# Kernel optimization log

Hardware: AMD Instinct MI355X
Metric: run time of the kernel (lower is better)

## Reference

```python
import jax, jax.numpy as jnp
import numpy as np

B, F = 512, 512
NUM_KERNEL, DIM_KERNEL = 50, 16


def setup_inputs() -> dict:
    key = jax.random.key(0)
    k1, k2 = jax.random.split(key)
    x = jax.random.normal(k1, (B, F), dtype=jnp.float32)
    # glorot-uniform-like scale for the learned kernel
    limit = (6.0 / (F + NUM_KERNEL * DIM_KERNEL)) ** 0.5
    W = jax.random.uniform(k2, (F, NUM_KERNEL * DIM_KERNEL), dtype=jnp.float32,
                           minval=-limit, maxval=limit)
    return {"x": x, "W": W}


def reference(x, W):
    # activation: (B, K, D)
    act = (x @ W).reshape(-1, NUM_KERNEL, DIM_KERNEL)
    # pairwise L1 over the kernel dim D: l1[b, b2, k] = sum_d |act[b,k,d] - act[b2,k,d]|
    diff = act[:, None, :, :] - act[None, :, :, :]      # (B, B, K, D)
    l1 = jnp.sum(jnp.abs(diff), axis=-1)                # (B, B, K)
    features = jnp.sum(jnp.exp(-l1), axis=1)            # (B, K), includes self-term (=1)
    return jnp.concatenate([x, features], axis=1)       # (B, F + K)
```

## Files before the change

kernel.cpp:

```cpp
#include <hip/hip_runtime.h>
#include <hip/hip_bf16.h>
#include <hip/hip_fp16.h>


#define B_ROWS 512
#define F_IN   512
#define NK     50
#define DK     16
#define N_COLS (NK * DK)
#define OUT_COLS (F_IN + NK)

#if __has_builtin(__builtin_amdgcn_exp2f)
#define EXP2F __builtin_amdgcn_exp2f
#else
#define EXP2F exp2f
#endif

typedef __attribute__((ext_vector_type(8))) short bf16x8;
typedef __attribute__((ext_vector_type(4))) float f32x4;

__device__ __forceinline__ short bfs(float f) {
    __hip_bfloat16 h = __float2bfloat16(f);
    return *reinterpret_cast<short*>(&h);
}

__global__ __launch_bounds__(256) void gemm_ksplit_kernel(const float* __restrict__ x,
                                                          const float* __restrict__ W,
                                                          float* __restrict__ act,
                                                          float* __restrict__ out) {
    __shared__ float red[4 * 64 * 8];

    const int tid = threadIdx.x;
    const int wave = tid >> 6, l = tid & 63;
    const int bid = blockIdx.y * 32 + blockIdx.x;

    if (bid < 128) {
        #pragma unroll
        for (int i = 0; i < 2; ++i) {
            int gid = bid * 512 + i * 256 + tid;
            int row = gid >> 7, c4 = gid & 127;
            float4 v = ((const float4*)x)[gid];
            float* o = out + row * OUT_COLS + c4 * 4;
            *(float2*)o = make_float2(v.x, v.y);
            *(float2*)(o + 2) = make_float2(v.z, v.w);
        }
    }

    const int mBase = blockIdx.x * 16;
    const int nBase = blockIdx.y * 32;
    const int rc = l & 15, kg = l >> 4;

    const float* pa = x + (mBase + rc) * F_IN + wave * 128 + kg * 8;
    const float* pb = W + (wave * 128 + kg * 8) * N_COLS + nBase + rc;

    f32x4 acc0 = {0.f, 0.f, 0.f, 0.f};
    f32x4 acc1 = {0.f, 0.f, 0.f, 0.f};

    #pragma unroll
    for (int ks = 0; ks < 4; ++ks) {
        float4 a0 = *(const float4*)(pa + ks * 32);
        float4 a1 = *(const float4*)(pa + ks * 32 + 4);
        bf16x8 a;
        a[0] = bfs(a0.x); a[1] = bfs(a0.y); a[2] = bfs(a0.z); a[3] = bfs(a0.w);
        a[4] = bfs(a1.x); a[5] = bfs(a1.y); a[6] = bfs(a1.z); a[7] = bfs(a1.w);

        const float* pk = pb + (ks * 32) * N_COLS;
        bf16x8 b0, b1;
        #pragma unroll
        for (int j = 0; j < 8; ++j) {
            b0[j] = bfs(pk[j * N_COLS]);
            b1[j] = bfs(pk[j * N_COLS + 16]);
        }
        acc0 = __builtin_amdgcn_mfma_f32_16x16x32_bf16(a, b0, acc0, 0, 0, 0);
        acc1 = __builtin_amdgcn_mfma_f32_16x16x32_bf16(a, b1, acc1, 0, 0, 0);
    }

    const int ro = (wave * 64 + l) * 8;
    *(f32x4*)(red + ro)     = acc0;
    *(f32x4*)(red + ro + 4) = acc1;
    __syncthreads();

    {
        const int e = tid * 2;
        const int le = e >> 3, j0 = e & 7;
        float2 s = make_float2(0.f, 0.f);
        #pragma unroll
        for (int w = 0; w < 4; ++w) {
            float2 v = *(const float2*)(red + w * 512 + e);
            s.x += v.x; s.y += v.y;
        }
        const int row = mBase + (le >> 4) * 4 + (j0 & 3);
        const int col = nBase + (le & 15) + (j0 >> 2) * 16;
        act[row * N_COLS + col]       = s.x;
        act[(row + 1) * N_COLS + col] = s.y;
    }
}

__global__ __launch_bounds__(256) void pairwise_h2_kernel(const float* __restrict__ act,
                                                          float* __restrict__ out) {
    const int k = blockIdx.x;
    const int chunk = blockIdx.y;
    __shared__ uint2 Ah4[B_ROWS * 4];

    const int tid = threadIdx.x;
    const float* base = act + k * DK;
    #pragma unroll
    for (int i = 0; i < 8; ++i) {
        int idx = tid + i * 256;
        int b = idx >> 2, d4 = idx & 3;
        float4 v = *(const float4*)(base + b * N_COLS + d4 * 4);
        __half2 h0 = __float22half2_rn(make_float2(v.x, v.y));
        __half2 h1 = __float22half2_rn(make_float2(v.z, v.w));
        uint2 u;
        u.x = __builtin_bit_cast(unsigned, h0);
        u.y = __builtin_bit_cast(unsigned, h1);
        Ah4[idx ^ ((idx >> 6) & 15)] = u;
    }
    __syncthreads();

    const int rt = tid >> 5;
    const int q = tid & 31;
    const int row0 = chunk * 32 + rt * 4;

    __half2 m[4][8];
    #pragma unroll
    for (int r = 0; r < 4; ++r) {
        int gr = row0 + r;
        int xr = (gr >> 4) & 15;
        #pragma unroll
        for (int j = 0; j < 4; ++j) {
            uint2 u = Ah4[(gr * 4 + j) ^ xr];
            m[r][2 * j]     = __builtin_bit_cast(__half2, u.x);
            m[r][2 * j + 1] = __builtin_bit_cast(__half2, u.y);
        }
    }

    const uint2* bq = Ah4 + q * 64;
    const int xm = q & 15;

    float acc[4] = {0.f, 0.f, 0.f, 0.f};
    #pragma unroll 4
    for (int i = 0; i < 16; ++i) {
        __half2 v[8];
        #pragma unroll
        for (int j = 0; j < 4; ++j) {
            uint2 u = bq[(i * 4 + j) ^ xm];
            v[2 * j]     = __builtin_bit_cast(__half2, u.x);
            v[2 * j + 1] = __builtin_bit_cast(__half2, u.y);
        }
        #pragma unroll
        for (int r = 0; r < 4; ++r) {
            __half2 s = __habs2(__hsub2(m[r][0], v[0]));
            #pragma unroll
            for (int jj = 1; jj < 8; ++jj)
                s = __hadd2(s, __habs2(__hsub2(m[r][jj], v[jj])));
            float2 f = __half22float2(s);
            acc[r] += EXP2F((f.x + f.y) * -1.4426950408889634f);
        }
    }

    #pragma unroll
    for (int r = 0; r < 4; ++r) {
        acc[r] += __shfl_xor(acc[r], 1);
        acc[r] += __shfl_xor(acc[r], 2);
        acc[r] += __shfl_xor(acc[r], 4);
        acc[r] += __shfl_xor(acc[r], 8);
        acc[r] += __shfl_xor(acc[r], 16);
    }
    if (q == 0) {
        #pragma unroll
        for (int r = 0; r < 4; ++r)
            out[(row0 + r) * OUT_COLS + F_IN + k] = acc[r];
    }
}

extern "C" void kernel_launch(void* const* d_in, const int* in_sizes, int n_in,
                              void* d_out, int out_size, void* d_ws, size_t ws_size,
                              hipStream_t stream) {
    const float* x = (const float*)d_in[0];
    const float* W = (const float*)d_in[1];
    float* out = (float*)d_out;
    float* act = (float*)d_ws;

    gemm_ksplit_kernel<<<dim3(32, 25), dim3(256), 0, stream>>>(x, W, act, out);
    pairwise_h2_kernel<<<dim3(50, 16), dim3(256), 0, stream>>>(act, out);
}
```

Baseline: 32.05 us.

## Fuse GEMM and pairwise kernels with ticket-based producer/consumer scheduling

Merges the two launches into a single persistent-style kernel. Blocks take tickets from a global atomic counter: the first 40 tickets compute larger 64x160 GEMM tiles over the full K (no k-split reduction) and write fp16 activations. Later tickets run the pairwise L1/exp work after spinning on per-column-group done counters. This removes one launch boundary, halves activation traffic by storing fp16, and lets the pairwise phase overlap with GEMM tail work. The cost is global atomics, spin-wait latency, bounded-spin correctness risk and much less GEMM parallelism (40 blocks).

```diff
diff --git a/kernel.cpp b/kernel.cpp
--- a/kernel.cpp
+++ b/kernel.cpp
@@ -9,6 +9,9 @@
 #define DK     16
 #define N_COLS (NK * DK)
 #define OUT_COLS (F_IN + NK)
+#define NBLOCKS 800
+#define NPROD   40
+#define POOL    (NPROD + NBLOCKS)
 
 #if __has_builtin(__builtin_amdgcn_exp2f)
 #define EXP2F __builtin_amdgcn_exp2f
@@ -19,102 +22,121 @@
 typedef __attribute__((ext_vector_type(8))) short bf16x8;
 typedef __attribute__((ext_vector_type(4))) float f32x4;
 
+__device__ unsigned long long g_ticket = 0;
+__device__ unsigned long long g_done[5] = {0, 0, 0, 0, 0};
+
 __device__ __forceinline__ short bfs(float f) {
     __hip_bfloat16 h = __float2bfloat16(f);
     return *reinterpret_cast<short*>(&h);
 }
 
-__global__ __launch_bounds__(256) void gemm_ksplit_kernel(const float* __restrict__ x,
-                                                          const float* __restrict__ W,
-                                                          float* __restrict__ act,
-                                                          float* __restrict__ out) {
-    __shared__ float red[4 * 64 * 8];
-
+__global__ __launch_bounds__(256) void fused_kernel(const float* __restrict__ x,
+                                                    const float* __restrict__ W,
+                                                    __half* __restrict__ act_h,
+                                                    float* __restrict__ out) {
+    __shared__ uint2 Ah4[2048];
+    __shared__ unsigned long long sTk;
+
+    const int bid = blockIdx.x;
     const int tid = threadIdx.x;
     const int wave = tid >> 6, l = tid & 63;
-    const int bid = blockIdx.y * 32 + blockIdx.x;
-
-    if (bid < 128) {
-        #pragma unroll
-        for (int i = 0; i < 2; ++i) {
-            int gid = bid * 512 + i * 256 + tid;
-            int row = gid >> 7, c4 = gid & 127;
-            float4 v = ((const float4*)x)[gid];
-            float* o = out + row * OUT_COLS + c4 * 4;
-            *(float2*)o = make_float2(v.x, v.y);
-            *(float2*)(o + 2) = make_float2(v.z, v.w);
-        }
-    }
-
-    const int mBase = blockIdx.x * 16;
-    const int nBase = blockIdx.y * 32;
     const int rc = l & 15, kg = l >> 4;
 
-    const float* pa = x + (mBase + rc) * F_IN + wave * 128 + kg * 8;
-    const float* pb = W + (wave * 128 + kg * 8) * N_COLS + nBase + rc;
-
-    f32x4 acc0 = {0.f, 0.f, 0.f, 0.f};
-    f32x4 acc1 = {0.f, 0.f, 0.f, 0.f};
-
-    #pragma unroll
-    for (int ks = 0; ks < 4; ++ks) {
-        float4 a0 = *(const float4*)(pa + ks * 32);
-        float4 a1 = *(const float4*)(pa + ks * 32 + 4);
-        bf16x8 a;
-        a[0] = bfs(a0.x); a[1] = bfs(a0.y); a[2] = bfs(a0.z); a[3] = bfs(a0.w);
-        a[4] = bfs(a1.x); a[5] = bfs(a1.y); a[6] = bfs(a1.z); a[7] = bfs(a1.w);
-
-        const float* pk = pb + (ks * 32) * N_COLS;
-        bf16x8 b0, b1;
-        #pragma unroll
-        for (int j = 0; j < 8; ++j) {
-            b0[j] = bfs(pk[j * N_COLS]);
-            b1[j] = bfs(pk[j * N_COLS + 16]);
-        }
-        acc0 = __builtin_amdgcn_mfma_f32_16x16x32_bf16(a, b0, acc0, 0, 0, 0);
-        acc1 = __builtin_amdgcn_mfma_f32_16x16x32_bf16(a, b1, acc1, 0, 0, 0);
-    }
-
-    const int ro = (wave * 64 + l) * 8;
-    *(f32x4*)(red + ro)     = acc0;
-    *(f32x4*)(red + ro + 4) = acc1;
+    unsigned long long epoch;
+    for (;;) {
+        __syncthreads();
+        if (tid == 0) sTk = atomicAdd(&g_ticket, 1ULL);
+        __syncthreads();
+        const unsigned long long t = sTk;
+        const unsigned r = (unsigned)(t % POOL);
+        if (r >= NPROD) { epoch = t / POOL; break; }
+
+        const int mc = r / 5, ncp = r % 5;
+        const int wm = (wave >> 1) & 1, wn = wave & 1;
+        const int rowb = mc * 64 + wm * 32;
+        const int colb = ncp * 160 + wn * 80;
+
+        const float* paw = x + (rowb + rc) * F_IN + kg * 8;
+        const float* pbw = W + (kg * 8) * N_COLS + colb + rc;
+
+        f32x4 acc[2][5] = {};
+        #pragma unroll 2
+        for (int ks = 0; ks < 16; ++ks) {
+            bf16x8 a[2];
+            #pragma unroll
+            for (int mf = 0; mf < 2; ++mf) {
+                float4 a0 = *(const float4*)(paw + mf * 16 * F_IN + ks * 32);
+                float4 a1 = *(const float4*)(paw + mf * 16 * F_IN + ks * 32 + 4);
+                a[mf][0] = bfs(a0.x); a[mf][1] = bfs(a0.y);
+                a[mf][2] = bfs(a0.z); a[mf][3] = bfs(a0.w);
+                a[mf][4] = bfs(a1.x); a[mf][5] = bfs(a1.y);
+                a[mf][6] = bfs(a1.z); a[mf][7] = bfs(a1.w);
+            }
+            const float* pk = pbw + ks * 32 * N_COLS;
+            #pragma unroll
+            for (int nf = 0; nf < 5; ++nf) {
+                bf16x8 b;
+                #pragma unroll
+                for (int j = 0; j < 8; ++j)
+                    b[j] = bfs(pk[j * N_COLS + nf * 16]);
+                acc[0][nf] = __builtin_amdgcn_mfma_f32_16x16x32_bf16(a[0], b, acc[0][nf], 0, 0, 0);
+                acc[1][nf] = __builtin_amdgcn_mfma_f32_16x16x32_bf16(a[1], b, acc[1][nf], 0, 0, 0);
+            }
+        }
+        #pragma unroll
+        for (int mf = 0; mf < 2; ++mf)
+            #pragma unroll
+            for (int nf = 0; nf < 5; ++nf)
+                #pragma unroll
+                for (int r4 = 0; r4 < 4; ++r4) {
+                    int row = rowb + mf * 16 + kg * 4 + r4;
+                    int col = colb + nf * 16 + rc;
+                    act_h[row * N_COLS + col] = __float2half(acc[mf][nf][r4]);
+                }
+
+        if (ncp == 0) {
+            #pragma unroll
+            for (int i = 0; i < 32; ++i) {
+                int idx = tid + i * 256;
+                int rr = idx >> 7, c4 = idx & 127;
+                float4 v = *(const float4*)(x + (mc * 64 + rr) * F_IN + c4 * 4);
+                float* o = out + (mc * 64 + rr) * OUT_COLS + c4 * 4;
+                *(float2*)o = make_float2(v.x, v.y);
+                *(float2*)(o + 2) = make_float2(v.z, v.w);
+            }
+        }
+
+        __syncthreads();
+        if (tid == 0) {
+            __builtin_amdgcn_fence(__ATOMIC_RELEASE, "");
+            __hip_atomic_fetch_add(&g_done[ncp], 1ULL,
+                                   __ATOMIC_RELAXED, __HIP_MEMORY_SCOPE_SYSTEM);
+        }
+    }
+
+    const int k = bid >> 4;
+    const int chunk = bid & 15;
+    const int nc = k / 10;
+    const unsigned long long target = 8ULL * (epoch + 1);
+
+    if (tid == 0) {
+        for (int it = 0; it < 3000000; ++it) {
+            if (__hip_atomic_load(&g_done[nc], __ATOMIC_RELAXED,
+                                  __HIP_MEMORY_SCOPE_SYSTEM) >= target) break;
+        }
+    }
     __syncthreads();
+    __builtin_amdgcn_fence(__ATOMIC_ACQUIRE, "");
 
     {
-        const int e = tid * 2;
-        const int le = e >> 3, j0 = e & 7;
-        float2 s = make_float2(0.f, 0.f);
-        #pragma unroll
-        for (int w = 0; w < 4; ++w) {
-            float2 v = *(const float2*)(red + w * 512 + e);
-            s.x += v.x; s.y += v.y;
-        }
-        const int row = mBase + (le >> 4) * 4 + (j0 & 3);
-        const int col = nBase + (le & 15) + (j0 >> 2) * 16;
-        act[row * N_COLS + col]       = s.x;
-        act[(row + 1) * N_COLS + col] = s.y;
-    }
-}
-
-__global__ __launch_bounds__(256) void pairwise_h2_kernel(const float* __restrict__ act,
-                                                          float* __restrict__ out) {
-    const int k = blockIdx.x;
-    const int chunk = blockIdx.y;
-    __shared__ uint2 Ah4[B_ROWS * 4];
-
-    const int tid = threadIdx.x;
-    const float* base = act + k * DK;
-    #pragma unroll
-    for (int i = 0; i < 8; ++i) {
-        int idx = tid + i * 256;
-        int b = idx >> 2, d4 = idx & 3;
-        float4 v = *(const float4*)(base + b * N_COLS + d4 * 4);
-        __half2 h0 = __float22half2_rn(make_float2(v.x, v.y));
-        __half2 h1 = __float22half2_rn(make_float2(v.z, v.w));
-        uint2 u;
-        u.x = __builtin_bit_cast(unsigned, h0);
-        u.y = __builtin_bit_cast(unsigned, h1);
-        Ah4[idx ^ ((idx >> 6) & 15)] = u;
+        const __half* base = act_h + k * DK;
+        #pragma unroll
+        for (int i = 0; i < 8; ++i) {
+            int idx = tid + i * 256;
+            int b = idx >> 2, d4 = idx & 3;
+            uint2 u = *(const uint2*)(base + b * N_COLS + d4 * 4);
+            Ah4[idx ^ ((idx >> 6) & 15)] = u;
+        }
     }
     __syncthreads();
 
@@ -180,8 +202,7 @@
     const float* x = (const float*)d_in[0];
     const float* W = (const float*)d_in[1];
     float* out = (float*)d_out;
-    float* act = (float*)d_ws;
-
-    gemm_ksplit_kernel<<<dim3(32, 25), dim3(256), 0, stream>>>(x, W, act, out);
-    pairwise_h2_kernel<<<dim3(50, 16), dim3(256), 0, stream>>>(act, out);
+    __half* act_h = (__half*)d_ws;
+
+    fused_kernel<<<dim3(NBLOCKS), dim3(256), 0, stream>>>(x, W, act_h, out);
 }
```

After: 70.73 us. 121% more time.

## Exploit pairwise symmetry with upper-triangular 32x32 tiles and atomic accumulation

Applied to the files above, without the earlier changes.

The pairwise kernel now works on upper-triangular 32x32 row-block tiles for each kernel k. Each off-diagonal tile adds its exp(-L1) sums to both the row and column outputs through atomics, which roughly halves the distance and exp work. The GEMM kernel zeroes the feature columns first so the atomics start from zero. In exchange, the launch grows to 6800 small blocks that each do little work, and the atomic adds make the summation order nondeterministic.

```diff
diff --git a/kernel.cpp b/kernel.cpp
--- a/kernel.cpp
+++ b/kernel.cpp
@@ -44,6 +44,10 @@
             *(float2*)o = make_float2(v.x, v.y);
             *(float2*)(o + 2) = make_float2(v.z, v.w);
         }
+    }
+    if (bid < 50) {
+        out[tid * OUT_COLS + F_IN + bid] = 0.f;
+        out[(tid + 256) * OUT_COLS + F_IN + bid] = 0.f;
     }
 
     const int mBase = blockIdx.x * 16;
@@ -96,81 +100,88 @@
     }
 }
 
-__global__ __launch_bounds__(256) void pairwise_h2_kernel(const float* __restrict__ act,
-                                                          float* __restrict__ out) {
-    const int k = blockIdx.x;
-    const int chunk = blockIdx.y;
-    __shared__ uint2 Ah4[B_ROWS * 4];
+__global__ __launch_bounds__(256) void pairwise_sym_kernel(const float* __restrict__ act,
+                                                           float* __restrict__ out) {
+    __shared__ uint2 St[256];
+    __shared__ float Jr[4][32];
 
+    const int p = blockIdx.x;
+    const int k = blockIdx.y;
     const int tid = threadIdx.x;
-    const float* base = act + k * DK;
-    #pragma unroll
-    for (int i = 0; i < 8; ++i) {
-        int idx = tid + i * 256;
-        int b = idx >> 2, d4 = idx & 3;
-        float4 v = *(const float4*)(base + b * N_COLS + d4 * 4);
+
+    int ci = 0, pp = p;
+    while (pp >= 16 - ci) { pp -= 16 - ci; ++ci; }
+    const int cj = ci + pp;
+    const bool diag = (ci == cj);
+
+    {
+        const int rl = tid >> 2, d4 = tid & 3;
+        const int grow = (rl < 32 ? ci * 32 + rl : cj * 32 + rl - 32);
+        float4 v = *(const float4*)(act + grow * N_COLS + k * DK + d4 * 4);
         __half2 h0 = __float22half2_rn(make_float2(v.x, v.y));
         __half2 h1 = __float22half2_rn(make_float2(v.z, v.w));
         uint2 u;
         u.x = __builtin_bit_cast(unsigned, h0);
         u.y = __builtin_bit_cast(unsigned, h1);
-        Ah4[idx ^ ((idx >> 6) & 15)] = u;
+        St[rl * 4 + d4] = u;
     }
     __syncthreads();
 
     const int rt = tid >> 5;
     const int q = tid & 31;
-    const int row0 = chunk * 32 + rt * 4;
 
-    __half2 m[4][8];
+    __half2 m[4][8], v[8];
     #pragma unroll
-    for (int r = 0; r < 4; ++r) {
-        int gr = row0 + r;
-        int xr = (gr >> 4) & 15;
+    for (int r = 0; r < 4; ++r)
         #pragma unroll
         for (int j = 0; j < 4; ++j) {
-            uint2 u = Ah4[(gr * 4 + j) ^ xr];
+            uint2 u = St[(rt * 4 + r) * 4 + j];
             m[r][2 * j]     = __builtin_bit_cast(__half2, u.x);
             m[r][2 * j + 1] = __builtin_bit_cast(__half2, u.y);
         }
+    #pragma unroll
+    for (int j = 0; j < 4; ++j) {
+        uint2 u = St[(32 + q) * 4 + j];
+        v[2 * j]     = __builtin_bit_cast(__half2, u.x);
+        v[2 * j + 1] = __builtin_bit_cast(__half2, u.y);
     }
 
-    const uint2* bq = Ah4 + q * 64;
-    const int xm = q & 15;
-
-    float acc[4] = {0.f, 0.f, 0.f, 0.f};
-    #pragma unroll 4
-    for (int i = 0; i < 16; ++i) {
-        __half2 v[8];
+    float e[4];
+    #pragma unroll
+    for (int r = 0; r < 4; ++r) {
+        __half2 s = __habs2(__hsub2(m[r][0], v[0]));
         #pragma unroll
-        for (int j = 0; j < 4; ++j) {
-            uint2 u = bq[(i * 4 + j) ^ xm];
-            v[2 * j]     = __builtin_bit_cast(__half2, u.x);
-            v[2 * j + 1] = __builtin_bit_cast(__half2, u.y);
-        }
-        #pragma unroll
-        for (int r = 0; r < 4; ++r) {
-            __half2 s = __habs2(__hsub2(m[r][0], v[0]));
-            #pragma unroll
-            for (int jj = 1; jj < 8; ++jj)
-                s = __hadd2(s, __habs2(__hsub2(m[r][jj], v[jj])));
-            float2 f = __half22float2(s);
-            acc[r] += EXP2F((f.x + f.y) * -1.4426950408889634f);
-        }
+        for (int jj = 1; jj < 8; ++jj)
+            s = __hadd2(s, __habs2(__hsub2(m[r][jj], v[jj])));
+        float2 f = __half22float2(s);
+        e[r] = EXP2F((f.x + f.y) * -1.4426950408889634f);
     }
 
+    float ai[4] = {e[0], e[1], e[2], e[3]};
     #pragma unroll
     for (int r = 0; r < 4; ++r) {
-        acc[r] += __shfl_xor(acc[r], 1);
-        acc[r] += __shfl_xor(acc[r], 2);
-        acc[r] += __shfl_xor(acc[r], 4);
-        acc[r] += __shfl_xor(acc[r], 8);
-        acc[r] += __shfl_xor(acc[r], 16);
+        ai[r] += __shfl_xor(ai[r], 1);
+        ai[r] += __shfl_xor(ai[r], 2);
+        ai[r] += __shfl_xor(ai[r], 4);
+        ai[r] += __shfl_xor(ai[r], 8);
+        ai[r] += __shfl_xor(ai[r], 16);
     }
     if (q == 0) {
         #pragma unroll
         for (int r = 0; r < 4; ++r)
-            out[(row0 + r) * OUT_COLS + F_IN + k] = acc[r];
+            atomicAdd(&out[(ci * 32 + rt * 4 + r) * OUT_COLS + F_IN + k], ai[r]);
+    }
+
+    if (!diag) {
+        float aj = (e[0] + e[1]) + (e[2] + e[3]);
+        aj += __shfl_xor(aj, 32);
+        const int wv = tid >> 6, l = tid & 63;
+        if (l < 32) Jr[wv][l] = aj;
+        __syncthreads();
+        if (tid < 32) {
+            float s = (Jr[0][tid] + Jr[1][tid]) + (Jr[2][tid] + Jr[3][tid]);
+            atomicAdd(&out[(cj * 32 + tid) * OUT_COLS + F_IN + k], s);
+        }
     }
 }
 
@@ -183,5 +194,5 @@
     float* act = (float*)d_ws;
 
     gemm_ksplit_kernel<<<dim3(32, 25), dim3(256), 0, stream>>>(x, W, act, out);
-    pairwise_h2_kernel<<<dim3(50, 16), dim3(256), 0, stream>>>(act, out);
+    pairwise_sym_kernel<<<dim3(136, 50), dim3(256), 0, stream>>>(act, out);
 }
```

Measured after the change: 48.96 us. 52.8% more time.
